# Kernel optimization log

Measured on AMD Instinct MI355X. Metric: run time of the kernel, lower is better.

Reference implementation:

```python
import math
import jax, jax.numpy as jnp
import numpy as np

N_NODES = 50_000
N_EDGES = 500_000
INPUT_DIM = 6
HIDDEN = 128
FREQS = 32
LN_EPS = 1e-5
TWO_PI = 2.0 * math.pi


def wrap_angle(a):
    return (a + math.pi) % (2.0 * math.pi) - math.pi


def setup_inputs() -> dict:
    key = jax.random.key(0)
    ks = jax.random.split(key, 12)
    source = jax.random.normal(ks[0], (N_NODES, 5), dtype=jnp.float32)
    target = jax.random.normal(ks[1], (N_NODES, 5), dtype=jnp.float32)
    edge = jax.random.randint(ks[2], (2, N_EDGES), 0, N_NODES, dtype=jnp.int64)
    K = 2 * FREQS + 1
    # FourierEmbedding params: freqs table + 6 per-dim MLPs (Linear->LN->ReLU->Linear), stacked over dim axis
    freqs = jax.random.normal(ks[3], (INPUT_DIM, FREQS), dtype=jnp.float32)
    W1 = jax.random.normal(ks[4], (INPUT_DIM, K, HIDDEN), dtype=jnp.float32) * (1.0 / math.sqrt(K))
    b1 = jnp.zeros((INPUT_DIM, HIDDEN), dtype=jnp.float32)
    ln_w = jnp.ones((INPUT_DIM, HIDDEN), dtype=jnp.float32)
    ln_b = jnp.zeros((INPUT_DIM, HIDDEN), dtype=jnp.float32)
    W2 = jax.random.normal(ks[5], (INPUT_DIM, HIDDEN, HIDDEN), dtype=jnp.float32) * (1.0 / math.sqrt(HIDDEN))
    b2 = jnp.zeros((INPUT_DIM, HIDDEN), dtype=jnp.float32)
    return {"source": source, "target": target, "edge": edge,
            "freqs": freqs, "W1": W1, "b1": b1, "ln_w": ln_w, "ln_b": ln_b,
            "W2": W2, "b2": b2}


def _compute_feature(source, target, edge):
    # source/target: [N, 5] = X, Y, Heading, Speed, (other)
    sp, sh, ss = source[:, :2], source[:, 2], source[:, 3]
    tp, th, ts = target[:, :2], target[:, 2], target[:, 3]
    src, tgt = edge[0], edge[1]
    pd = sp[src] - tp[tgt]                         # [E, 2]
    dx, dy = pd[:, 0], pd[:, 1]
    dist = jnp.sqrt(dx * dx + dy * dy)
    is_close = (dist < 3.0).astype(pd.dtype)
    ang = jnp.arctan2(dy, dx)
    dh = wrap_angle(sh[src] - th[tgt])
    cos_a, sin_a = jnp.cos(ang), jnp.sin(ang)
    tvx, tvy = ts * jnp.cos(th), ts * jnp.sin(th)
    t_close = tvx[tgt] * cos_a + tvy[tgt] * sin_a
    svx, svy = ss * jnp.cos(sh), ss * jnp.sin(sh)
    s_close = svx[src] * cos_a + svy[src] * sin_a
    return jnp.stack([dx, dy, dh, is_close, t_close, s_close], axis=-1)  # [E, 6]


def _fourier_embed(feat, freqs, W1, b1, ln_w, ln_b, W2, b2):
    # feat: [E, 6]; freqs: [6, F]
    x = feat[:, :, None] * freqs[None, :, :] * TWO_PI          # [E, 6, F]
    x = jnp.concatenate([jnp.cos(x), jnp.sin(x), feat[:, :, None]], axis=-1)  # [E, 6, 2F+1]
    h = jnp.einsum('edk,dkh->edh', x, W1) + b1[None]           # [E, 6, H]
    mu = h.mean(axis=-1, keepdims=True)
    var = jnp.mean((h - mu) ** 2, axis=-1, keepdims=True)
    h = (h - mu) * jax.lax.rsqrt(var + LN_EPS) * ln_w[None] + ln_b[None]
    h = jax.nn.relu(h)
    out = jnp.einsum('edh,dhg->edg', h, W2) + b2[None]         # [E, 6, H]
    return out.sum(axis=1)                                     # [E, H]


def reference(source, target, edge, freqs, W1, b1, ln_w, ln_b, W2, b2):
    feat = jax.lax.stop_gradient(_compute_feature(source, target, edge))  # torch.no_grad()
    return _fourier_embed(feat, freqs, W1, b1, ln_w, ln_b, W2, b2)
```

## Files before the change

kernel.cpp:

```cpp
#include <hip/hip_runtime.h>
#include <hip/hip_bf16.h>
#include <math.h>

#define E_EDGES 500000
#define PI_F 3.14159265358979323846f
#define TWOPI_F 6.28318530717958647692f

typedef __attribute__((ext_vector_type(4))) float f32x4;
typedef __attribute__((ext_vector_type(8))) short s16x8;

static __device__ __forceinline__ short f2bf(float x) {
    __hip_bfloat16 h = __float2bfloat16(x);
    return __builtin_bit_cast(short, h);
}

__global__ void rape_prep_kernel(const float* __restrict__ W1,
                                 const float* __restrict__ W2,
                                 s16x8* __restrict__ ws)
{
    const int d  = blockIdx.x / 24;
    const int sg = blockIdx.x % 24;
    const int j  = threadIdx.x;
    s16x8 v;
    if (sg < 8) {
        const float* W1d = W1 + (size_t)d * 65 * 128;
        const int kb = (sg >> 2) * 32 + (sg & 3) * 4;
        #pragma unroll
        for (int i = 0; i < 4; ++i) {
            v[i]     = f2bf(W1d[(kb + i) * 128 + j]);
            v[i + 4] = f2bf(W1d[(kb + 16 + i) * 128 + j]);
        }
    } else {
        const int sg2 = sg - 8;
        const float* W2d = W2 + (size_t)d * 128 * 128;
        const int kb = (sg2 >> 2) * 32 + (sg2 & 3) * 4;
        #pragma unroll
        for (int i = 0; i < 4; ++i) {
            v[i]     = f2bf(W2d[(kb + i) * 128 + j]);
            v[i + 4] = f2bf(W2d[(kb + 16 + i) * 128 + j]);
        }
    }
    ws[(size_t)d * 24 * 128 + sg * 128 + j] = v;
}

__global__ __launch_bounds__(256, 3)
void rape_mfma10_kernel(const float* __restrict__ source,
                        const float* __restrict__ target,
                        const int*   __restrict__ edge,
                        const float* __restrict__ freqs,
                        const float* __restrict__ W1,
                        const float* __restrict__ b1,
                        const float* __restrict__ ln_w,
                        const float* __restrict__ ln_b,
                        const float* __restrict__ b2,
                        const s16x8* __restrict__ wsg,
                        float* __restrict__ out)
{
    __shared__ s16x8 slabA[8 * 128];
    __shared__ s16x8 slabB[8 * 128];
    __shared__ float feat_s[6][128];
    __shared__ float b1_s[768];
    __shared__ float lnw_s[768];
    __shared__ float lnb_s[768];
    __shared__ float w164_s[768];
    __shared__ float freq_s[192];

    const int tid   = threadIdx.x;
    const int lane  = tid & 63;
    const int wv    = tid >> 6;
    const int c     = lane & 15;
    const int g     = lane >> 4;
    const int ebase = blockIdx.x * 128;

    for (int i = tid; i < 768; i += 256) {
        b1_s[i]   = b1[i];
        lnw_s[i]  = ln_w[i];
        lnb_s[i]  = ln_b[i];
        w164_s[i] = W1[((size_t)(i >> 7) * 65 + 64) * 128 + (i & 127)];
    }
    if (tid < 192) freq_s[tid] = freqs[tid];

    if (tid < 128) {
        int ec = ebase + tid; if (ec >= E_EDGES) ec = E_EDGES - 1;
        int si = edge[ec];
        int ti = edge[E_EDGES + ec];
        const float* S = source + (size_t)si * 5;
        const float* T = target + (size_t)ti * 5;
        float spx = S[0], spy = S[1], shd = S[2], ss = S[3];
        float tpx = T[0], tpy = T[1], thd = T[2], ts = T[3];
        float dx = spx - tpx, dy = spy - tpy;
        float dist = sqrtf(dx * dx + dy * dy);
        float ic  = dist < 3.0f ? 1.0f : 0.0f;
        float inv = dist > 0.0f ? 1.0f / dist : 0.0f;
        float ca  = dist > 0.0f ? dx * inv : 1.0f;
        float sa  = dy * inv;
        float a = shd - thd + PI_F;
        float r = fmodf(a, TWOPI_F);
        r = r < 0.0f ? r + TWOPI_F : r;
        float dh = r - PI_F;
        float tc = ts * (cosf(thd) * ca + sinf(thd) * sa);
        float sc = ss * (cosf(shd) * ca + sinf(shd) * sa);
        feat_s[0][tid] = dx; feat_s[1][tid] = dy; feat_s[2][tid] = dh;
        feat_s[3][tid] = ic; feat_s[4][tid] = tc; feat_s[5][tid] = sc;
    }

    f32x4 acc[2][8];
    #pragma unroll
    for (int gt = 0; gt < 8; ++gt) {
        f32x4 s = {0.f, 0.f, 0.f, 0.f};
        #pragma unroll
        for (int d = 0; d < 6; ++d)
            s += *(const f32x4*)(b2 + d * 128 + gt * 16 + g * 4);
        acc[0][gt] = s; acc[1][gt] = s;
    }

    for (int d = 0; d < 6; ++d) {
        __syncthreads();

        {
            const char* gsrc = (const char*)(wsg + (size_t)d * 24 * 128);
            #pragma unroll
            for (int it = 0; it < 4; ++it) {
                const int off = tid * 16 + it * 4096;
                __builtin_amdgcn_global_load_lds(
                    (const __attribute__((address_space(1))) unsigned int*)(gsrc + off),
                    (__attribute__((address_space(3))) unsigned int*)((char*)slabA + off),
                    16, 0, 0);
            }
            #pragma unroll
            for (int it = 0; it < 4; ++it) {
                const int off = tid * 16 + it * 4096;
                __builtin_amdgcn_global_load_lds(
                    (const __attribute__((address_space(1))) unsigned int*)(gsrc + 16384 + off),
                    (__attribute__((address_space(3))) unsigned int*)((char*)slabB + off),
                    16, 0, 0);
            }
        }

        s16x8 bfr[2][2];
        float xv[2];
        const f32x4 fq0 = *(const f32x4*)(freq_s + d * 32 + g * 4);
        const f32x4 fq1 = *(const f32x4*)(freq_s + d * 32 + 16 + g * 4);
        #pragma unroll
        for (int es = 0; es < 2; ++es) {
            const float x = feat_s[d][wv * 32 + es * 16 + c];
            xv[es] = x;
            s16x8 bc, bs;
            #pragma unroll
            for (int i = 0; i < 8; ++i) {
                const float f = (i < 4) ? fq0[i] : fq1[i - 4];
                const float t = x * f;
                const float tf = t - floorf(t);
                bc[i] = f2bf(__builtin_amdgcn_cosf(tf));
                bs[i] = f2bf(__builtin_amdgcn_sinf(tf));
            }
            bfr[es][0] = bc; bfr[es][1] = bs;
        }

        f32x4 d1[2][8];
        #pragma unroll
        for (int jt = 0; jt < 8; ++jt) {
            const f32x4 bv  = *(const f32x4*)(b1_s   + d * 128 + jt * 16 + g * 4);
            const f32x4 wv4 = *(const f32x4*)(w164_s + d * 128 + jt * 16 + g * 4);
            d1[0][jt] = bv + xv[0] * wv4;
            d1[1][jt] = bv + xv[1] * wv4;
        }

        __syncthreads();

        #pragma unroll
        for (int jt = 0; jt < 8; ++jt) {
            const s16x8 a0 = slabA[(0 + g) * 128 + jt * 16 + c];
            const s16x8 a1 = slabA[(4 + g) * 128 + jt * 16 + c];
            #pragma unroll
            for (int es = 0; es < 2; ++es) {
                d1[es][jt] = __builtin_amdgcn_mfma_f32_16x16x32_bf16(a0, bfr[es][0], d1[es][jt], 0, 0, 0);
                d1[es][jt] = __builtin_amdgcn_mfma_f32_16x16x32_bf16(a1, bfr[es][1], d1[es][jt], 0, 0, 0);
            }
        }

        float mu[2], rinv[2];
        #pragma unroll
        for (int es = 0; es < 2; ++es) {
            float s1 = 0.f, s2 = 0.f;
            #pragma unroll
            for (int jt = 0; jt < 8; ++jt)
                #pragma unroll
                for (int q = 0; q < 4; ++q) {
                    const float v = d1[es][jt][q];
                    s1 += v; s2 = fmaf(v, v, s2);
                }
            s1 += __shfl_xor(s1, 16); s1 += __shfl_xor(s1, 32);
            s2 += __shfl_xor(s2, 16); s2 += __shfl_xor(s2, 32);
            mu[es] = s1 * 0.0078125f;
            const float var = s2 * 0.0078125f - mu[es] * mu[es];
            rinv[es] = rsqrtf(var + 1e-5f);
        }
        s16x8 pb[2][4];
        #pragma unroll
        for (int ks = 0; ks < 4; ++ks) {
            #pragma unroll
            for (int p = 0; p < 2; ++p) {
                const int jt = 2 * ks + p;
                const f32x4 lw = *(const f32x4*)(lnw_s + d * 128 + jt * 16 + g * 4);
                const f32x4 lb = *(const f32x4*)(lnb_s + d * 128 + jt * 16 + g * 4);
                #pragma unroll
                for (int es = 0; es < 2; ++es) {
                    #pragma unroll
                    for (int q = 0; q < 4; ++q) {
                        float hv = (d1[es][jt][q] - mu[es]) * rinv[es];
                        hv = fmaf(hv, lw[q], lb[q]);
                        hv = fmaxf(hv, 0.f);
                        pb[es][ks][q + 4 * p] = f2bf(hv);
                    }
                }
            }
        }

        __syncthreads();

        {
            const char* gsrc = (const char*)(wsg + (size_t)d * 24 * 128) + 32768;
            #pragma unroll
            for (int it = 0; it < 4; ++it) {
                const int off = tid * 16 + it * 4096;
                __builtin_amdgcn_global_load_lds(
                    (const __attribute__((address_space(1))) unsigned int*)(gsrc + off),
                    (__attribute__((address_space(3))) unsigned int*)((char*)slabA + off),
                    16, 0, 0);
            }
        }

        #pragma unroll
        for (int ks = 0; ks < 2; ++ks) {
            #pragma unroll
            for (int gt = 0; gt < 8; ++gt) {
                const s16x8 a = slabB[(ks * 4 + g) * 128 + gt * 16 + c];
                #pragma unroll
                for (int es = 0; es < 2; ++es)
                    acc[es][gt] = __builtin_amdgcn_mfma_f32_16x16x32_bf16(a, pb[es][ks], acc[es][gt], 0, 0, 0);
            }
        }

        __syncthreads();

        #pragma unroll
        for (int ks = 2; ks < 4; ++ks) {
            #pragma unroll
            for (int gt = 0; gt < 8; ++gt) {
                const s16x8 a = slabA[((ks - 2) * 4 + g) * 128 + gt * 16 + c];
                #pragma unroll
                for (int es = 0; es < 2; ++es)
                    acc[es][gt] = __builtin_amdgcn_mfma_f32_16x16x32_bf16(a, pb[es][ks], acc[es][gt], 0, 0, 0);
            }
        }
    }

    #pragma unroll
    for (int es = 0; es < 2; ++es) {
        const int e = ebase + wv * 32 + es * 16 + c;
        if (e < E_EDGES) {
            float* op = out + (size_t)e * 128 + g * 4;
            #pragma unroll
            for (int gt = 0; gt < 8; ++gt)
                *(f32x4*)(op + gt * 16) = acc[es][gt];
        }
    }
}

extern "C" void kernel_launch(void* const* d_in, const int* in_sizes, int n_in,
                              void* d_out, int out_size, void* d_ws, size_t ws_size,
                              hipStream_t stream) {
    const float* source = (const float*)d_in[0];
    const float* target = (const float*)d_in[1];
    const int*   edge   = (const int*)  d_in[2];
    const float* freqs  = (const float*)d_in[3];
    const float* W1     = (const float*)d_in[4];
    const float* b1     = (const float*)d_in[5];
    const float* ln_w   = (const float*)d_in[6];
    const float* ln_b   = (const float*)d_in[7];
    const float* W2     = (const float*)d_in[8];
    const float* b2     = (const float*)d_in[9];
    float* out = (float*)d_out;
    s16x8* wsg = (s16x8*)d_ws;

    rape_prep_kernel<<<6 * 24, 128, 0, stream>>>(W1, W2, wsg);

    const int nblocks = (E_EDGES + 127) / 128;
    rape_mfma10_kernel<<<nblocks, 256, 0, stream>>>(
        source, target, edge, freqs, W1, b1, ln_w, ln_b, b2, wsg, out);
}
```

Before: 284.5 us.

## Double-buffer W1 slabs, load full W2 slab at once, pack params as bf16

```diff
diff --git a/kernel.cpp b/kernel.cpp
--- a/kernel.cpp
+++ b/kernel.cpp
@@ -8,10 +8,17 @@
 
 typedef __attribute__((ext_vector_type(4))) float f32x4;
 typedef __attribute__((ext_vector_type(8))) short s16x8;
+typedef __attribute__((ext_vector_type(4))) unsigned int u32x4;
 
 static __device__ __forceinline__ short f2bf(float x) {
     __hip_bfloat16 h = __float2bfloat16(x);
     return __builtin_bit_cast(short, h);
+}
+static __device__ __forceinline__ float bf_lo(unsigned u) {
+    return __builtin_bit_cast(float, u << 16);
+}
+static __device__ __forceinline__ float bf_hi(unsigned u) {
+    return __builtin_bit_cast(float, u & 0xFFFF0000u);
 }
 
 __global__ void rape_prep_kernel(const float* __restrict__ W1,
@@ -43,8 +50,8 @@
     ws[(size_t)d * 24 * 128 + sg * 128 + j] = v;
 }
 
-__global__ __launch_bounds__(256, 3)
-void rape_mfma10_kernel(const float* __restrict__ source,
+__global__ __launch_bounds__(256, 2)
+void rape_mfma11_kernel(const float* __restrict__ source,
                         const float* __restrict__ target,
                         const int*   __restrict__ edge,
                         const float* __restrict__ freqs,
@@ -56,13 +63,11 @@
                         const s16x8* __restrict__ wsg,
                         float* __restrict__ out)
 {
-    __shared__ s16x8 slabA[8 * 128];
-    __shared__ s16x8 slabB[8 * 128];
+    __shared__ s16x8 w1buf[2][8 * 128];
+    __shared__ s16x8 w2buf[16 * 128];
     __shared__ float feat_s[6][128];
-    __shared__ float b1_s[768];
-    __shared__ float lnw_s[768];
-    __shared__ float lnb_s[768];
-    __shared__ float w164_s[768];
+    __shared__ unsigned b1w_s[768];
+    __shared__ unsigned lnwb_s[768];
     __shared__ float freq_s[192];
 
     const int tid   = threadIdx.x;
@@ -73,10 +78,12 @@
     const int ebase = blockIdx.x * 128;
 
     for (int i = tid; i < 768; i += 256) {
-        b1_s[i]   = b1[i];
-        lnw_s[i]  = ln_w[i];
-        lnb_s[i]  = ln_b[i];
-        w164_s[i] = W1[((size_t)(i >> 7) * 65 + 64) * 128 + (i & 127)];
+        unsigned ub = (unsigned short)f2bf(b1[i]);
+        unsigned uw = (unsigned short)f2bf(W1[((size_t)(i >> 7) * 65 + 64) * 128 + (i & 127)]);
+        b1w_s[i] = ub | (uw << 16);
+        unsigned ulw = (unsigned short)f2bf(ln_w[i]);
+        unsigned ulb = (unsigned short)f2bf(ln_b[i]);
+        lnwb_s[i] = ulw | (ulb << 16);
     }
     if (tid < 192) freq_s[tid] = freqs[tid];
 
@@ -104,6 +111,18 @@
         feat_s[3][tid] = ic; feat_s[4][tid] = tc; feat_s[5][tid] = sc;
     }
 
+    {
+        const char* gsrc = (const char*)wsg;
+        #pragma unroll
+        for (int it = 0; it < 4; ++it) {
+            const int off = tid * 16 + it * 4096;
+            __builtin_amdgcn_global_load_lds(
+                (const __attribute__((address_space(1))) unsigned int*)(gsrc + off),
+                (__attribute__((address_space(3))) unsigned int*)((char*)w1buf[0] + off),
+                16, 0, 0);
+        }
+    }
+
     f32x4 acc[2][8];
     #pragma unroll
     for (int gt = 0; gt < 8; ++gt) {
@@ -118,21 +137,13 @@
         __syncthreads();
 
         {
-            const char* gsrc = (const char*)(wsg + (size_t)d * 24 * 128);
-            #pragma unroll
-            for (int it = 0; it < 4; ++it) {
+            const char* gsrc = (const char*)(wsg + (size_t)d * 24 * 128) + 16384;
+            #pragma unroll
+            for (int it = 0; it < 8; ++it) {
                 const int off = tid * 16 + it * 4096;
                 __builtin_amdgcn_global_load_lds(
                     (const __attribute__((address_space(1))) unsigned int*)(gsrc + off),
-                    (__attribute__((address_space(3))) unsigned int*)((char*)slabA + off),
-                    16, 0, 0);
-            }
-            #pragma unroll
-            for (int it = 0; it < 4; ++it) {
-                const int off = tid * 16 + it * 4096;
-                __builtin_amdgcn_global_load_lds(
-                    (const __attribute__((address_space(1))) unsigned int*)(gsrc + 16384 + off),
-                    (__attribute__((address_space(3))) unsigned int*)((char*)slabB + off),
+                    (__attribute__((address_space(3))) unsigned int*)((char*)w2buf + off),
                     16, 0, 0);
             }
         }
@@ -160,22 +171,38 @@
         f32x4 d1[2][8];
         #pragma unroll
         for (int jt = 0; jt < 8; ++jt) {
-            const f32x4 bv  = *(const f32x4*)(b1_s   + d * 128 + jt * 16 + g * 4);
-            const f32x4 wv4 = *(const f32x4*)(w164_s + d * 128 + jt * 16 + g * 4);
-            d1[0][jt] = bv + xv[0] * wv4;
-            d1[1][jt] = bv + xv[1] * wv4;
+            const u32x4 pw = *(const u32x4*)(b1w_s + d * 128 + jt * 16 + g * 4);
+            #pragma unroll
+            for (int q = 0; q < 4; ++q) {
+                const float bv  = bf_lo(pw[q]);
+                const float wv4 = bf_hi(pw[q]);
+                d1[0][jt][q] = fmaf(xv[0], wv4, bv);
+                d1[1][jt][q] = fmaf(xv[1], wv4, bv);
+            }
         }
 
         __syncthreads();
 
         #pragma unroll
         for (int jt = 0; jt < 8; ++jt) {
-            const s16x8 a0 = slabA[(0 + g) * 128 + jt * 16 + c];
-            const s16x8 a1 = slabA[(4 + g) * 128 + jt * 16 + c];
+            const s16x8 a0 = w1buf[d & 1][(0 + g) * 128 + jt * 16 + c];
+            const s16x8 a1 = w1buf[d & 1][(4 + g) * 128 + jt * 16 + c];
             #pragma unroll
             for (int es = 0; es < 2; ++es) {
                 d1[es][jt] = __builtin_amdgcn_mfma_f32_16x16x32_bf16(a0, bfr[es][0], d1[es][jt], 0, 0, 0);
                 d1[es][jt] = __builtin_amdgcn_mfma_f32_16x16x32_bf16(a1, bfr[es][1], d1[es][jt], 0, 0, 0);
+            }
+        }
+
+        if (d < 5) {
+            const char* gsrc = (const char*)(wsg + (size_t)(d + 1) * 24 * 128);
+            #pragma unroll
+            for (int it = 0; it < 4; ++it) {
+                const int off = tid * 16 + it * 4096;
+                __builtin_amdgcn_global_load_lds(
+                    (const __attribute__((address_space(1))) unsigned int*)(gsrc + off),
+                    (__attribute__((address_space(3))) unsigned int*)((char*)w1buf[(d + 1) & 1] + off),
+                    16, 0, 0);
             }
         }
 
@@ -196,20 +223,22 @@
             const float var = s2 * 0.0078125f - mu[es] * mu[es];
             rinv[es] = rsqrtf(var + 1e-5f);
         }
+
         s16x8 pb[2][4];
         #pragma unroll
         for (int ks = 0; ks < 4; ++ks) {
             #pragma unroll
             for (int p = 0; p < 2; ++p) {
                 const int jt = 2 * ks + p;
-                const f32x4 lw = *(const f32x4*)(lnw_s + d * 128 + jt * 16 + g * 4);
-                const f32x4 lb = *(const f32x4*)(lnb_s + d * 128 + jt * 16 + g * 4);
+                const u32x4 lnp = *(const u32x4*)(lnwb_s + d * 128 + jt * 16 + g * 4);
                 #pragma unroll
                 for (int es = 0; es < 2; ++es) {
                     #pragma unroll
                     for (int q = 0; q < 4; ++q) {
+                        const float lw = bf_lo(lnp[q]);
+                        const float lb = bf_hi(lnp[q]);
                         float hv = (d1[es][jt][q] - mu[es]) * rinv[es];
-                        hv = fmaf(hv, lw[q], lb[q]);
+                        hv = fmaf(hv, lw, lb);
                         hv = fmaxf(hv, 0.f);
                         pb[es][ks][q + 4 * p] = f2bf(hv);
                     }
@@ -217,38 +246,11 @@
             }
         }
 
-        __syncthreads();
-
-        {
-            const char* gsrc = (const char*)(wsg + (size_t)d * 24 * 128) + 32768;
-            #pragma unroll
-            for (int it = 0; it < 4; ++it) {
-                const int off = tid * 16 + it * 4096;
-                __builtin_amdgcn_global_load_lds(
-                    (const __attribute__((address_space(1))) unsigned int*)(gsrc + off),
-                    (__attribute__((address_space(3))) unsigned int*)((char*)slabA + off),
-                    16, 0, 0);
-            }
-        }
-
-        #pragma unroll
-        for (int ks = 0; ks < 2; ++ks) {
+        #pragma unroll
+        for (int ks = 0; ks < 4; ++ks) {
             #pragma unroll
             for (int gt = 0; gt < 8; ++gt) {
-                const s16x8 a = slabB[(ks * 4 + g) * 128 + gt * 16 + c];
-                #pragma unroll
-                for (int es = 0; es < 2; ++es)
-                    acc[es][gt] = __builtin_amdgcn_mfma_f32_16x16x32_bf16(a, pb[es][ks], acc[es][gt], 0, 0, 0);
-            }
-        }
-
-        __syncthreads();
-
-        #pragma unroll
-        for (int ks = 2; ks < 4; ++ks) {
-            #pragma unroll
-            for (int gt = 0; gt < 8; ++gt) {
-                const s16x8 a = slabA[((ks - 2) * 4 + g) * 128 + gt * 16 + c];
+                const s16x8 a = w2buf[(ks * 4 + g) * 128 + gt * 16 + c];
                 #pragma unroll
                 for (int es = 0; es < 2; ++es)
                     acc[es][gt] = __builtin_amdgcn_mfma_f32_16x16x32_bf16(a, pb[es][ks], acc[es][gt], 0, 0, 0);
@@ -287,6 +289,6 @@
     rape_prep_kernel<<<6 * 24, 128, 0, stream>>>(W1, W2, wsg);
 
     const int nblocks = (E_EDGES + 127) / 128;
-    rape_mfma10_kernel<<<nblocks, 256, 0, stream>>>(
+    rape_mfma11_kernel<<<nblocks, 256, 0, stream>>>(
         source, target, edge, freqs, W1, b1, ln_w, ln_b, b2, wsg, out);
 }
```

Result: faster. 258.9 us (-9.0%).
